# Performance work log

Measured on AMD Instinct MI355X. Metric: run time of the kernel, lower is better.

## Reference

```python
import jax, jax.numpy as jnp
import numpy as np
from jax import lax

# FPN anchor layout: 800x800 image, 3 anchors/loc, strides 4,8,16,32,64
LEVEL_ANCHORS = [120000, 30000, 7500, 1875, 507]
PRE_NMS_TOP_N = 1000   # per level (test mode)
POST_NMS_TOP_N = 1000
NMS_THRESH = 0.7
MIN_SIZE = 1e-3


def setup_inputs() -> dict:
    key = jax.random.key(0)
    k1, k2, k3, k4 = jax.random.split(key, 4)
    A = sum(LEVEL_ANCHORS)
    bs = 2
    predicts = jax.random.normal(k1, (bs, A, 4), jnp.float32) * 0.1
    objectness = jax.random.normal(k2, (bs, A, 1), jnp.float32)
    cxy = jax.random.uniform(k3, (A, 2), jnp.float32, 0.0, 800.0)
    wh = jax.random.uniform(k4, (A, 2), jnp.float32, 16.0, 128.0)
    anchors = jnp.concatenate([cxy - 0.5 * wh, cxy + 0.5 * wh], axis=-1)
    valid_size = jnp.full((bs, 2), 800.0, jnp.float32)  # (w, h) per image
    return {"predicts": predicts, "objectness": objectness,
            "anchors": anchors, "valid_size": valid_size}


def _decode(predicts, anchors):
    # BoxCoder.decoder with weights [1,1,1,1]
    awh = anchors[:, 2:] - anchors[:, :2]          # [A,2]
    axy = anchors[:, :2] + 0.5 * awh               # [A,2]
    xy = axy + predicts[..., :2] * awh             # [bs,A,2] center
    wh = jnp.exp(predicts[..., 2:]) * awh          # [bs,A,2]
    x1y1 = xy - 0.5 * wh
    return jnp.concatenate([x1y1, x1y1 + wh], axis=-1)  # [bs,A,4]


def _per_level_topk_idx(scores):
    # scores: [bs, A] -> concat of per-level top-k indices (global anchor ids)
    idx_list, offset = [], 0
    for n in LEVEL_ANCHORS:
        k = min(PRE_NMS_TOP_N, n)
        _, top = lax.top_k(scores[:, offset:offset + n], k)
        idx_list.append(top + offset)
        offset += n
    return jnp.concatenate(idx_list, axis=1)  # [bs, K]


def _nms_keep(boxes, valid, thresh):
    # boxes sorted by score desc; returns boolean keep mask (sequential NMS)
    x1, y1, x2, y2 = boxes[:, 0], boxes[:, 1], boxes[:, 2], boxes[:, 3]
    area = (x2 - x1) * (y2 - y1)
    xx1 = jnp.maximum(x1[:, None], x1[None, :])
    yy1 = jnp.maximum(y1[:, None], y1[None, :])
    xx2 = jnp.minimum(x2[:, None], x2[None, :])
    yy2 = jnp.minimum(y2[:, None], y2[None, :])
    inter = jnp.maximum(xx2 - xx1, 0.0) * jnp.maximum(yy2 - yy1, 0.0)
    iou = inter / (area[:, None] + area[None, :] - inter + 1e-9)
    sup = iou > thresh                                   # [N,N]
    N = boxes.shape[0]
    ar = jnp.arange(N)

    def body(i, keep):
        suppressed = jnp.any((ar < i) & keep & sup[i])
        return keep.at[i].set(keep[i] & ~suppressed)

    return lax.fori_loop(0, N, body, valid)


def _filter_image(boxes, scores, lvls, wh):
    # boxes [K,4], scores [K], lvls [K] int, wh [2]=(w,h)
    w, h = wh[0], wh[1]
    x1 = jnp.clip(boxes[:, 0], 0.0, w)
    y1 = jnp.clip(boxes[:, 1], 0.0, h)
    x2 = jnp.clip(boxes[:, 2], 0.0, w)
    y2 = jnp.clip(boxes[:, 3], 0.0, h)
    boxes = jnp.stack([x1, y1, x2, y2], axis=-1)
    valid = (x2 - x1 > MIN_SIZE) & (y2 - y1 > MIN_SIZE)
    s = jnp.where(valid, scores, -jnp.inf)
    order = jnp.argsort(-s)
    boxes, s, lvls, valid = boxes[order], s[order], lvls[order], valid[order]
    # batched_nms: offset each level into a disjoint coordinate range
    max_coord = lax.stop_gradient(jnp.max(boxes)) + 1.0
    off = lvls.astype(boxes.dtype) * max_coord
    keep = _nms_keep(lax.stop_gradient(boxes) + off[:, None], valid, NMS_THRESH)
    # take first POST_NMS_TOP_N kept (boxes are score-sorted)
    rank = jnp.cumsum(keep) - 1
    slot = jnp.where(keep & (rank < POST_NMS_TOP_N), rank, POST_NMS_TOP_N)
    out_b = jnp.zeros((POST_NMS_TOP_N + 1, 4), boxes.dtype).at[slot].set(boxes)[:POST_NMS_TOP_N]
    out_s = jnp.zeros((POST_NMS_TOP_N + 1,), s.dtype).at[slot].set(
        jnp.where(keep, s, 0.0))[:POST_NMS_TOP_N]
    return out_b, out_s


def reference(predicts, objectness, anchors, valid_size):
    bs = predicts.shape[0]
    proposals = _decode(predicts, anchors)            # [bs,A,4]
    scores = objectness[..., 0]                       # [bs,A]
    idx = _per_level_topk_idx(scores)                 # [bs,K]
    bidx = jnp.arange(bs)[:, None]
    boxes = proposals[bidx, idx]                      # [bs,K,4]
    sc = scores[bidx, idx]                            # [bs,K]
    levels_all = jnp.concatenate(
        [jnp.full((n,), i, jnp.int32) for i, n in enumerate(LEVEL_ANCHORS)])
    lvl = levels_all[idx]                             # [bs,K]
    final_boxes, final_scores = jax.vmap(_filter_image)(boxes, sc, lvl, valid_size)
    return final_boxes, final_scores
```

## Files before the change

### kernel.cpp

```cpp
#include <hip/hip_runtime.h>

typedef unsigned int u32;
typedef unsigned long long u64;

#define A_TOT    159882
#define BS       2
#define KTOP     1000
#define CAND_CAP 4096
#define HB       4096
#define ABLK     4096
#define NBH      40
#define EPT      16

static const size_t HIST12_OFF   = 0;
static const size_t CUT_OFF      = 131072;
static const size_t CCNT_OFF     = 131104;
static const size_t MAXC_OFF     = 131136;
static const size_t NV_OFF       = 131144;
static const size_t CHUNKANY_OFF = 131200;
static const size_t ZERO_END     = 132480;
static const size_t CAND_OFF     = 132480;
static const size_t LKEY2_OFF    = 394624;
static const size_t LBOX_OFF     = 476544;
static const size_t LSC_OFF      = 640384;
static const size_t RANK_OFF     = 681344;
static const size_t MASK_OFF     = 759168;

__device__ __forceinline__ int level_of(int a) {
  if (a < 120000) return 0;
  if (a < 150000) return 1;
  if (a < 157500) return 2;
  if (a < 159375) return 3;
  return 4;
}

__device__ __forceinline__ u32 dkey(float s) {
  u32 b = __float_as_uint(s);
  return (b & 0x80000000u) ? b : (~b & 0x7FFFFFFFu);
}

__device__ __forceinline__ void decode_clip(const float* __restrict__ pred,
                                            const float* __restrict__ anch,
                                            const float* __restrict__ vs,
                                            int b, int a,
                                            float& x1c, float& y1c, float& x2c, float& y2c,
                                            bool& valid) {
  const float* pp = pred + ((size_t)b * A_TOT + (size_t)a) * 4;
  const float* aa = anch + (size_t)a * 4;
  float ax1 = aa[0], ay1 = aa[1], ax2 = aa[2], ay2 = aa[3];
  float px = pp[0], py = pp[1], pw = pp[2], ph = pp[3];
  float aw  = __fsub_rn(ax2, ax1);
  float ah  = __fsub_rn(ay2, ay1);
  float acx = __fadd_rn(ax1, __fmul_rn(0.5f, aw));
  float acy = __fadd_rn(ay1, __fmul_rn(0.5f, ah));
  float cx  = __fadd_rn(acx, __fmul_rn(px, aw));
  float cy  = __fadd_rn(acy, __fmul_rn(py, ah));
  float w   = __fmul_rn(expf(pw), aw);
  float h   = __fmul_rn(expf(ph), ah);
  float x1  = __fsub_rn(cx, __fmul_rn(0.5f, w));
  float y1  = __fsub_rn(cy, __fmul_rn(0.5f, h));
  float x2  = __fadd_rn(x1, w);
  float y2  = __fadd_rn(y1, h);
  float Wv = vs[b * 2 + 0], Hv = vs[b * 2 + 1];
  x1c = fminf(fmaxf(x1, 0.0f), Wv);
  y1c = fminf(fmaxf(y1, 0.0f), Hv);
  x2c = fminf(fmaxf(x2, 0.0f), Wv);
  y2c = fminf(fmaxf(y2, 0.0f), Hv);
  valid = (__fsub_rn(x2c, x1c) > 0.001f) && (__fsub_rn(y2c, y1c) > 0.001f);
}

__device__ __forceinline__ void bitonic_u64(u64* arr, int N, int t, int nt) {
  for (int k = 2; k <= N; k <<= 1) {
    for (int j = k >> 1; j > 0; j >>= 1) {
      __syncthreads();
      for (int i = t; i < N; i += nt) {
        int ixj = i ^ j;
        if (ixj > i) {
          u64 x = arr[i], y = arr[ixj];
          bool up = ((i & k) == 0);
          if (up ? (x > y) : (x < y)) { arr[i] = y; arr[ixj] = x; }
        }
      }
    }
  }
  __syncthreads();
}

__device__ __forceinline__ int lbound(const u64* __restrict__ arr, int n, u64 key) {
  int lo = 0, hi = n;
  while (lo < hi) { int mid = (lo + hi) >> 1; if (arr[mid] < key) lo = mid + 1; else hi = mid; }
  return lo;
}

__global__ void k_zero(char* __restrict__ ws) {
  size_t i = (size_t)blockIdx.x * blockDim.x + threadIdx.x;
  if (i * 4 < ZERO_END) ((u32*)ws)[i] = 0u;
}

__global__ void k_hist12(const float* __restrict__ obj, char* __restrict__ ws) {
  __shared__ u32 h[2 * HB];
  int tid = threadIdx.x;
  int b = blockIdx.x / NBH, loc = blockIdx.x % NBH;
  int start = loc * ABLK;
  int l0 = level_of(start);
  if (l0 >= 4) return;
  for (int i = tid; i < 2 * HB; i += 256) h[i] = 0u;
  __syncthreads();
  for (int it = 0; it < EPT; ++it) {
    int a = start + it * 256 + tid;
    if (a < A_TOT) {
      int l = level_of(a);
      if (l < 4) {
        u32 d = dkey(obj[(size_t)b * A_TOT + a]);
        atomicAdd(&h[(u32)(l - l0) * HB + (d >> 20)], 1u);
      }
    }
  }
  __syncthreads();
  int lend = level_of(min(start + ABLK - 1, A_TOT - 1));
  int nseg = ((l0 + 1 <= lend) && (l0 + 1 < 4)) ? 2 : 1;
  for (int s = 0; s < nseg; ++s) {
    u32* gh = (u32*)(ws + HIST12_OFF) + (size_t)(b * 4 + l0 + s) * HB;
    for (int i = tid; i < HB; i += 256) {
      u32 v = h[s * HB + i];
      if (v) atomicAdd(&gh[i], v);
    }
  }
}

__global__ void k_compactsel(const float* __restrict__ obj, char* __restrict__ ws) {
  __shared__ u32 scan[256];
  __shared__ u32 cutv[2];
  __shared__ u32 lcnt[2], gbase[2];
  int tid = threadIdx.x, lane = tid & 63;
  int b = blockIdx.x / NBH, loc = blockIdx.x % NBH;
  int start = loc * ABLK;
  int l0 = level_of(start);
  if (l0 >= 4) return;
  int lend = level_of(min(start + ABLK - 1, A_TOT - 1));
  int nseg = ((l0 + 1 <= lend) && (l0 + 1 < 4)) ? 2 : 1;
  if (tid < 2) lcnt[tid] = 0;
  for (int s = 0; s < nseg; ++s) {
    int seg = b * 4 + l0 + s;
    const u32* gh = (const u32*)(ws + HIST12_OFF) + (size_t)seg * HB;
    u32 vals[16]; u32 acc = 0;
    for (int q = 0; q < 16; ++q) { vals[q] = gh[tid * 16 + q]; acc += vals[q]; }
    __syncthreads();
    scan[tid] = acc; __syncthreads();
    for (int d = 1; d < 256; d <<= 1) {
      u32 x = (tid >= d) ? scan[tid - d] : 0u; __syncthreads();
      scan[tid] += x; __syncthreads();
    }
    u32 incl = scan[tid], prev = incl - acc;
    if (prev < KTOP && incl >= KTOP) {
      u32 run = prev; int cb = HB - 1;
      for (int q = 0; q < 16; ++q) { run += vals[q]; if (run >= KTOP) { cb = tid * 16 + q; break; } }
      cutv[s] = (u32)cb;
      ((u32*)(ws + CUT_OFF))[seg] = (u32)cb;
    }
  }
  __syncthreads();
  u32 dv[EPT], slotv[EPT], passm = 0, sim = 0;
  for (int it = 0; it < EPT; ++it) {
    int a = start + it * 256 + tid;
    bool pass = false; u32 si = 0, d = 0;
    if (a < A_TOT) {
      int l = level_of(a);
      if (l < 4) {
        si = (u32)(l - l0);
        d = dkey(obj[(size_t)b * A_TOT + a]);
        pass = (d >> 20) <= cutv[si];
      }
    }
    dv[it] = d;
    u64 mp = __ballot(pass);
    u64 m1 = __ballot(pass && si == 1);
    u64 m0 = mp & ~m1;
    u32 slot = 0;
    if (m0) {
      int ld = __builtin_ctzll(m0);
      u32 wb = 0;
      if (lane == ld) wb = atomicAdd(&lcnt[0], (u32)__popcll(m0));
      wb = __shfl(wb, ld);
      if (pass && si == 0) slot = wb + (u32)__popcll(m0 & ((1ull << lane) - 1ull));
    }
    if (m1) {
      int ld = __builtin_ctzll(m1);
      u32 wb = 0;
      if (lane == ld) wb = atomicAdd(&lcnt[1], (u32)__popcll(m1));
      wb = __shfl(wb, ld);
      if (pass && si == 1) slot = wb + (u32)__popcll(m1 & ((1ull << lane) - 1ull));
    }
    slotv[it] = slot;
    if (pass) { passm |= 1u << it; if (si) sim |= 1u << it; }
  }
  __syncthreads();
  if (tid < 2)
    gbase[tid] = lcnt[tid] ? atomicAdd((u32*)(ws + CCNT_OFF) + (b * 4 + l0 + tid), lcnt[tid]) : 0u;
  __syncthreads();
  for (int it = 0; it < EPT; ++it) {
    if ((passm >> it) & 1u) {
      int a = start + it * 256 + tid;
      u32 si = (sim >> it) & 1u;
      int seg = b * 4 + l0 + (int)si;
      u32 gslot = gbase[si] + slotv[it];
      if (gslot < CAND_CAP)
        ((u64*)(ws + CAND_OFF))[(size_t)seg * CAND_CAP + gslot] =
            ((u64)dv[it] << 32) | (u32)a;
    }
  }
}

__global__ void k_sortdec(const float* __restrict__ pred, const float* __restrict__ obj,
                          const float* __restrict__ anch, const float* __restrict__ vs,
                          char* __restrict__ ws) {
  __shared__ u64 arr[CAND_CAP];
  __shared__ float4 dboxL[1024];
  __shared__ float dscL[1024];
  __shared__ u64 vmask[16];
  __shared__ u32 h8[256];
  __shared__ u32 auxv[4];
  int tid = threadIdx.x, lane = tid & 63, wv = tid >> 6;
  int P = blockIdx.x, b = P / 5, l = P % 5;
  int n;
  if (l == 4) {
    n = 507;
    for (int i = tid; i < 512; i += 256) {
      u64 v = ~0ull;
      if (i < 507) { int a = 159375 + i; v = ((u64)dkey(obj[(size_t)b * A_TOT + a]) << 32) | (u32)a; }
      arr[i] = v;
    }
    bitonic_u64(arr, 512, tid, 256);
  } else {
    n = KTOP;
    int seg = b * 4 + l;
    u32 cnt = min(((const u32*)(ws + CCNT_OFF))[seg], (u32)CAND_CAP);
    u32 cut12 = ((const u32*)(ws + CUT_OFF))[seg];
    const u64* cand = (const u64*)(ws + CAND_OFF) + (size_t)seg * CAND_CAP;
    int N;
    if (cnt <= 2048) {
      u64 ev[8];
      for (int j = 0; j < 8; ++j) { int idx = j * 256 + tid; ev[j] = (idx < (int)cnt) ? cand[idx] : ~0ull; }
      h8[tid] = 0;
      if (tid < 4) auxv[tid] = 0;
      __syncthreads();
      u32 myb = 0;
      for (int j = 0; j < 8; ++j) {
        int idx = j * 256 + tid;
        if (idx < (int)cnt) {
          u32 b12 = (u32)(ev[j] >> 52);
          if (b12 < cut12) myb++;
          else atomicAdd(&h8[(u32)(ev[j] >> 44) & 0xFFu], 1u);
        }
      }
      for (int off = 32; off; off >>= 1) myb += __shfl_xor(myb, off);
      if (lane == 0) atomicAdd(&auxv[0], myb);
      __syncthreads();
      u32 cntb = auxv[0];
      u32 hv = h8[tid];
      __syncthreads();
      for (int d = 1; d < 256; d <<= 1) {
        u32 x = (tid >= d) ? h8[tid - d] : 0u; __syncthreads();
        h8[tid] += x; __syncthreads();
      }
      u32 incl = h8[tid], excl = incl - hv;
      if (cntb + incl >= KTOP && cntb + excl < KTOP) { auxv[2] = (u32)tid; auxv[3] = cntb + incl; }
      __syncthreads();
      u32 cut20 = auxv[2]; u32 selt = auxv[3];
      for (int i = tid; i < 2048; i += 256) arr[i] = ~0ull;
      __syncthreads();
      for (int j = 0; j < 8; ++j) {
        int idx = j * 256 + tid;
        if (idx < (int)cnt) {
          u32 b12 = (u32)(ev[j] >> 52);
          bool sel = (b12 < cut12) || (((u32)(ev[j] >> 44) & 0xFFu) <= cut20);
          if (sel) { u32 p = atomicAdd(&auxv[1], 1u); arr[p] = ev[j]; }
        }
      }
      __syncthreads();
      N = 1024; while (N < (int)selt) N <<= 1;
    } else {
      for (int i = tid; i < CAND_CAP; i += 256) arr[i] = (i < (int)cnt) ? cand[i] : ~0ull;
      N = 1024; while (N < (int)cnt) N <<= 1;
    }
    bitonic_u64(arr, N, tid, 256);
  }
  float m = 0.0f;
  for (int k = 0; k < 4; ++k) {
    int j = k * 256 + tid;
    bool vb = false;
    if (j < n) {
      u64 key = arr[j];
      int a = (int)(u32)key;
      float x1, y1, x2, y2; bool valid;
      decode_clip(pred, anch, vs, b, a, x1, y1, x2, y2, valid);
      m = fmaxf(m, fmaxf(fmaxf(x1, y1), fmaxf(x2, y2)));
      dboxL[j] = make_float4(x1, y1, x2, y2);
      dscL[j] = obj[(size_t)b * A_TOT + a];
      vb = valid;
    }
    u64 bal = __ballot(vb);
    if (lane == 0) vmask[k * 4 + wv] = bal;
  }
  for (int off = 32; off; off >>= 1) m = fmaxf(m, __shfl_xor(m, off));
  if (lane == 0) atomicMax((u32*)(ws + MAXC_OFF) + b, __float_as_uint(m));
  __syncthreads();
  if (tid < 64) {
    int base = 0;
    for (int j0 = 0; j0 < n; j0 += 64) {
      int j = j0 + lane;
      bool v = (j < n) && ((vmask[j0 >> 6] >> lane) & 1ull);
      u64 mm = __ballot(v);
      int r = base + __popcll(mm & ((1ull << lane) - 1ull));
      if (v) {
        ((u64*)(ws + LKEY2_OFF))[(size_t)P * 1024 + r] = arr[j];
        ((float4*)(ws + LBOX_OFF))[(size_t)P * 1024 + r] = dboxL[j];
        ((float*)(ws + LSC_OFF))[(size_t)P * 1024 + r] = dscL[j];
      }
      base += __popcll(mm);
    }
    if (lane == 0) ((u32*)(ws + NV_OFF))[P] = (u32)base;
  }
}

__global__ void k_maskrank(char* __restrict__ ws) {
  int tid = threadIdx.x, bid = blockIdx.x;
  if (bid < 10) {
    int P = bid, b = P / 5, l = P % 5;
    int nv = (int)((const u32*)(ws + NV_OFF))[P];
    const u64* lkey = (const u64*)(ws + LKEY2_OFF);
    const u32* nvp = (const u32*)(ws + NV_OFF);
    for (int i = tid; i < nv; i += 256) {
      u64 key = lkey[(size_t)P * 1024 + i];
      int r = i;
      for (int l2 = 0; l2 < 5; ++l2) {
        if (l2 == l) continue;
        int P2 = b * 5 + l2;
        r += lbound(lkey + (size_t)P2 * 1024, (int)nvp[P2], key);
      }
      ((u32*)(ws + RANK_OFF))[(size_t)P * 1024 + i] = (u32)r;
    }
  }
  int idx = bid * 256 + tid;
  int w = idx & 15;
  int i = (idx >> 4) & 1023;
  int P = idx >> 14;
  if (P >= 10) return;
  int b = P / 5, l = P % 5;
  int n = (int)((const u32*)(ws + NV_OFF))[P];
  int W = (n + 63) >> 6;
  if (i >= n || w >= W) return;
  float M = __uint_as_float(((const u32*)(ws + MAXC_OFF))[b]);
  float maxc = __fadd_rn(M, 1.0f);
  float off = __fmul_rn((float)l, maxc);
  const float4* lbox = (const float4*)(ws + LBOX_OFF) + (size_t)P * 1024;
  float4 bi = lbox[i];
  bi.x = __fadd_rn(bi.x, off); bi.y = __fadd_rn(bi.y, off);
  bi.z = __fadd_rn(bi.z, off); bi.w = __fadd_rn(bi.w, off);
  float ai = __fmul_rn(__fsub_rn(bi.z, bi.x), __fsub_rn(bi.w, bi.y));
  u64 word = 0;
  int j0 = w << 6;
  int jn = min(64, n - j0);
  for (int jj = 0; jj < jn; ++jj) {
    float4 bj = lbox[j0 + jj];
    bj.x = __fadd_rn(bj.x, off); bj.y = __fadd_rn(bj.y, off);
    bj.z = __fadd_rn(bj.z, off); bj.w = __fadd_rn(bj.w, off);
    float xx1 = fmaxf(bi.x, bj.x);
    float yy1 = fmaxf(bi.y, bj.y);
    float xx2 = fminf(bi.z, bj.z);
    float yy2 = fminf(bi.w, bj.w);
    float iw = fmaxf(__fsub_rn(xx2, xx1), 0.0f);
    float ih = fmaxf(__fsub_rn(yy2, yy1), 0.0f);
    float inter = __fmul_rn(iw, ih);
    float aj = __fmul_rn(__fsub_rn(bj.z, bj.x), __fsub_rn(bj.w, bj.y));
    float den = __fadd_rn(__fsub_rn(__fadd_rn(ai, aj), inter), 1e-9f);
    float iou = __fdiv_rn(inter, den);
    if (iou > 0.7f) word |= (1ull << jj);
  }
  if (i >= j0 && i < j0 + 64) word &= ~(1ull << (i - j0));
  ((u64*)(ws + MASK_OFF))[(size_t)P * 16000 + (size_t)i * W + w] = word;
  if (word)
    atomicOr((u64*)(ws + CHUNKANY_OFF) + (size_t)P * 16 + (i >> 6), 1ull << (i & 63));
}

__global__ __launch_bounds__(320)
void k_scanfin(float* __restrict__ out, char* __restrict__ ws) {
  __shared__ u64 keeps[5][16];
  __shared__ u64 kb[80];
  __shared__ u32 sb[128];
  __shared__ u32 pfx[80];
  __shared__ u32 nvs[5];
  int tid = threadIdx.x, w = tid >> 6, lane = tid & 63;
  int b = blockIdx.x;
  for (int i = tid; i < 80; i += 320) kb[i] = 0ull;
  for (int i = tid; i < 4000; i += 320) out[(size_t)b * 4000 + i] = 0.0f;
  for (int i = tid; i < 1000; i += 320) out[8000 + (size_t)b * 1000 + i] = 0.0f;
  if (tid < 5) nvs[tid] = ((const u32*)(ws + NV_OFF))[b * 5 + tid];

  int P = b * 5 + w;
  int n = (int)((const u32*)(ws + NV_OFF))[P];
  int W = (n + 63) >> 6;
  const u64* maskg = (const u64*)(ws + MASK_OFF) + (size_t)P * 16000;
  u64 ca = (lane < 16) ? ((const u64*)(ws + CHUNKANY_OFF))[(size_t)P * 16 + lane] : 0ull;
  u64 dpre[16];
#pragma unroll
  for (int c = 0; c < 16; ++c) {
    int row = (c << 6) + lane;
    dpre[c] = (c < W && row < n) ? maskg[(size_t)row * W + c] : 0ull;
  }
  u64 removed = 0ull, keepw = 0ull;
#pragma unroll
  for (int c = 0; c < 16; ++c) {
    if (c >= W) break;
    int rb = c << 6;
    int rows = min(64, n - rb);
    u64 rowsmask = (rows == 64) ? ~0ull : ((1ull << rows) - 1ull);
    u64 curw = __shfl(removed, c);
    u64 cand = ~curw & rowsmask;
    u64 ca_c = __shfl(ca, c);
    u64 keptbits;
    u64 anyrows = ca_c & cand;
    if (anyrows == 0ull) {
      keptbits = cand;
    } else {
      u64 diag = dpre[c];
      u64 diagnz = __ballot(diag != 0ull) & cand;
      if (diagnz == 0ull) {
        keptbits = cand;
      } else {
        u64 remw = curw | ~rowsmask;
        u64 kept = 0ull;
        int pos = 0;
        u64 work = diagnz;
        while (work) {
          int s = __builtin_ctzll(work); work &= work - 1;
          u64 range = (1ull << s) - (1ull << pos);
          kept |= ~remw & range;
          bool k = ((remw >> s) & 1ull) == 0ull;
          u64 dr = __shfl(diag, s);
          if (k) { kept |= 1ull << s; remw |= dr; }
          pos = s + 1;
        }
        u64 tail = (pos >= 64) ? 0ull : (~0ull << pos);
        kept |= ~remw & tail & rowsmask;
        keptbits = kept;
      }
      u64 todo = keptbits & ca_c;
      while (todo) {
        int r0 = __builtin_ctzll(todo); todo &= todo - 1;
        int r1 = -1, r2 = -1, r3 = -1;
        if (todo) { r1 = __builtin_ctzll(todo); todo &= todo - 1; }
        if (todo) { r2 = __builtin_ctzll(todo); todo &= todo - 1; }
        if (todo) { r3 = __builtin_ctzll(todo); todo &= todo - 1; }
        u64 v0 = 0, v1 = 0, v2 = 0, v3 = 0;
        if (lane < W) {
          v0 = maskg[(size_t)(rb + r0) * W + lane];
          if (r1 >= 0) v1 = maskg[(size_t)(rb + r1) * W + lane];
          if (r2 >= 0) v2 = maskg[(size_t)(rb + r2) * W + lane];
          if (r3 >= 0) v3 = maskg[(size_t)(rb + r3) * W + lane];
        }
        removed |= v0 | v1 | v2 | v3;
      }
    }
    if (lane == c) keepw |= keptbits;
  }
  if (lane < 16) keeps[w][lane] = keepw;
  __syncthreads();

  const u32* rank = (const u32*)(ws + RANK_OFF);
  for (int idx = tid; idx < 5120; idx += 320) {
    int p = idx >> 10, i = idx & 1023;
    if (i < (int)nvs[p] && ((keeps[p][i >> 6] >> (i & 63)) & 1ull)) {
      u32 r = rank[(size_t)(b * 5 + p) * 1024 + i];
      atomicOr(&kb[r >> 6], 1ull << (r & 63));
    }
  }
  __syncthreads();
  if (tid < 128) sb[tid] = (tid < 80) ? (u32)__popcll(kb[tid]) : 0u;
  __syncthreads();
  for (int d = 1; d < 128; d <<= 1) {
    u32 x = (tid < 128 && tid >= d) ? sb[tid - d] : 0u;
    __syncthreads();
    if (tid < 128) sb[tid] += x;
    __syncthreads();
  }
  if (tid < 80) pfx[tid] = sb[tid] - (u32)__popcll(kb[tid]);
  __syncthreads();
  for (int idx = tid; idx < 5120; idx += 320) {
    int p = idx >> 10, i = idx & 1023;
    if (i < (int)nvs[p] && ((keeps[p][i >> 6] >> (i & 63)) & 1ull)) {
      int Pp = b * 5 + p;
      u32 r = rank[(size_t)Pp * 1024 + i];
      u64 word = kb[r >> 6];
      int slot = (int)pfx[r >> 6] + __popcll(word & ((1ull << (r & 63)) - 1ull));
      if (slot < KTOP) {
        float4 bx = ((const float4*)(ws + LBOX_OFF))[(size_t)Pp * 1024 + i];
        float s = ((const float*)(ws + LSC_OFF))[(size_t)Pp * 1024 + i];
        float* ob = out + ((size_t)b * KTOP + slot) * 4;
        ob[0] = bx.x; ob[1] = bx.y; ob[2] = bx.z; ob[3] = bx.w;
        out[8000 + (size_t)b * KTOP + slot] = s;
      }
    }
  }
}

extern "C" void kernel_launch(void* const* d_in, const int* in_sizes, int n_in,
                              void* d_out, int out_size, void* d_ws, size_t ws_size,
                              hipStream_t stream) {
  const float* pred = (const float*)d_in[0];
  const float* obj  = (const float*)d_in[1];
  const float* anch = (const float*)d_in[2];
  const float* vs   = (const float*)d_in[3];
  float* out = (float*)d_out;
  char* ws = (char*)d_ws;
  (void)in_sizes; (void)n_in; (void)out_size; (void)ws_size;

  int gZ = (int)((ZERO_END / 4 + 255) / 256);
  k_zero      <<<gZ,        256, 0, stream>>>(ws);
  k_hist12    <<<BS * NBH,  256, 0, stream>>>(obj, ws);
  k_compactsel<<<BS * NBH,  256, 0, stream>>>(obj, ws);
  k_sortdec   <<<10,        256, 0, stream>>>(pred, obj, anch, vs, ws);
  k_maskrank  <<<640,       256, 0, stream>>>(ws);
  k_scanfin   <<<2,         320, 0, stream>>>(out, ws);
}
```

Measured before the change: 194.6 us.

## Replace shared-memory bitonic with register/shuffle bitonic sort of 2048 keys

The per-level candidate sort in k_sortdec now keeps 8 keys per thread in registers. It uses in-register compare-swaps for small strides, wavefront shuffles for mid strides and shared memory only for strides of 512 and above. This replaces the histogram-based prefilter and the shared-memory bitonic sort, cutting barriers and LDS traffic. The trade-off is that every segment with at most 2048 candidates now always sorts a full 2048 elements, and the last level pads 507 keys to 2048, which adds compare work.

Measured after the change: 193.8 us. No clear change (-0.4%).

```diff
diff --git a/kernel.cpp b/kernel.cpp
--- a/kernel.cpp
+++ b/kernel.cpp
@@ -86,10 +86,58 @@
   __syncthreads();
 }
 
-__device__ __forceinline__ int lbound(const u64* __restrict__ arr, int n, u64 key) {
-  int lo = 0, hi = n;
-  while (lo < hi) { int mid = (lo + hi) >> 1; if (arr[mid] < key) lo = mid + 1; else hi = mid; }
-  return lo;
+__device__ __forceinline__ u64 shfl_xor_u64(u64 x, int lanemask) {
+  u32 lo = (u32)x, hi = (u32)(x >> 32);
+  lo = (u32)__shfl_xor((int)lo, lanemask);
+  hi = (u32)__shfl_xor((int)hi, lanemask);
+  return ((u64)hi << 32) | (u64)lo;
+}
+
+__device__ __forceinline__ void regsort2048(u64 v[8], int tid, u64* arr) {
+  for (int k = 2; k <= 2048; k <<= 1) {
+    for (int j = k >> 1; j > 0; j >>= 1) {
+      if (j >= 512) {
+        __syncthreads();
+#pragma unroll
+        for (int e = 0; e < 8; ++e) arr[tid * 8 + e] = v[e];
+        __syncthreads();
+#pragma unroll
+        for (int e = 0; e < 8; ++e) {
+          int i = tid * 8 + e, p = i ^ j;
+          u64 o = arr[p];
+          bool up = ((i & k) == 0);
+          bool keepmin = ((i < p) == up);
+          v[e] = keepmin ? (v[e] < o ? v[e] : o) : (v[e] > o ? v[e] : o);
+        }
+      } else if (j >= 8) {
+        int dl = j >> 3;
+#pragma unroll
+        for (int e = 0; e < 8; ++e) {
+          int i = tid * 8 + e;
+          u64 o = shfl_xor_u64(v[e], dl);
+          bool up = ((i & k) == 0);
+          bool keepmin = (((tid & dl) == 0) == up);
+          v[e] = keepmin ? (v[e] < o ? v[e] : o) : (v[e] > o ? v[e] : o);
+        }
+      } else {
+#pragma unroll
+        for (int e = 0; e < 8; ++e) {
+          int pe = e ^ j;
+          if (pe > e) {
+            int i = tid * 8 + e;
+            bool up = ((i & k) == 0);
+            u64 a = v[e], b2 = v[pe];
+            bool sw = up ? (a > b2) : (a < b2);
+            if (sw) { v[e] = b2; v[pe] = a; }
+          }
+        }
+      }
+    }
+  }
+  __syncthreads();
+#pragma unroll
+  for (int e = 0; e < 8; ++e) arr[tid * 8 + e] = v[e];
+  __syncthreads();
 }
 
 __global__ void k_zero(char* __restrict__ ws) {
@@ -218,72 +266,39 @@
   __shared__ float4 dboxL[1024];
   __shared__ float dscL[1024];
   __shared__ u64 vmask[16];
-  __shared__ u32 h8[256];
-  __shared__ u32 auxv[4];
   int tid = threadIdx.x, lane = tid & 63, wv = tid >> 6;
   int P = blockIdx.x, b = P / 5, l = P % 5;
   int n;
   if (l == 4) {
     n = 507;
-    for (int i = tid; i < 512; i += 256) {
-      u64 v = ~0ull;
-      if (i < 507) { int a = 159375 + i; v = ((u64)dkey(obj[(size_t)b * A_TOT + a]) << 32) | (u32)a; }
-      arr[i] = v;
-    }
-    bitonic_u64(arr, 512, tid, 256);
+    u64 v[8];
+#pragma unroll
+    for (int e = 0; e < 8; ++e) {
+      int idx = tid * 8 + e;
+      if (idx < 507) {
+        int a = 159375 + idx;
+        v[e] = ((u64)dkey(obj[(size_t)b * A_TOT + a]) << 32) | (u32)a;
+      } else v[e] = ~0ull;
+    }
+    regsort2048(v, tid, arr);
   } else {
     n = KTOP;
     int seg = b * 4 + l;
     u32 cnt = min(((const u32*)(ws + CCNT_OFF))[seg], (u32)CAND_CAP);
-    u32 cut12 = ((const u32*)(ws + CUT_OFF))[seg];
     const u64* cand = (const u64*)(ws + CAND_OFF) + (size_t)seg * CAND_CAP;
-    int N;
     if (cnt <= 2048) {
-      u64 ev[8];
-      for (int j = 0; j < 8; ++j) { int idx = j * 256 + tid; ev[j] = (idx < (int)cnt) ? cand[idx] : ~0ull; }
-      h8[tid] = 0;
-      if (tid < 4) auxv[tid] = 0;
-      __syncthreads();
-      u32 myb = 0;
-      for (int j = 0; j < 8; ++j) {
-        int idx = j * 256 + tid;
-        if (idx < (int)cnt) {
-          u32 b12 = (u32)(ev[j] >> 52);
-          if (b12 < cut12) myb++;
-          else atomicAdd(&h8[(u32)(ev[j] >> 44) & 0xFFu], 1u);
-        }
-      }
-      for (int off = 32; off; off >>= 1) myb += __shfl_xor(myb, off);
-      if (lane == 0) atomicAdd(&auxv[0], myb);
-      __syncthreads();
-      u32 cntb = auxv[0];
-      u32 hv = h8[tid];
-      __syncthreads();
-      for (int d = 1; d < 256; d <<= 1) {
-        u32 x = (tid >= d) ? h8[tid - d] : 0u; __syncthreads();
-        h8[tid] += x; __syncthreads();
-      }
-      u32 incl = h8[tid], excl = incl - hv;
-      if (cntb + incl >= KTOP && cntb + excl < KTOP) { auxv[2] = (u32)tid; auxv[3] = cntb + incl; }
-      __syncthreads();
-      u32 cut20 = auxv[2]; u32 selt = auxv[3];
-      for (int i = tid; i < 2048; i += 256) arr[i] = ~0ull;
-      __syncthreads();
-      for (int j = 0; j < 8; ++j) {
-        int idx = j * 256 + tid;
-        if (idx < (int)cnt) {
-          u32 b12 = (u32)(ev[j] >> 52);
-          bool sel = (b12 < cut12) || (((u32)(ev[j] >> 44) & 0xFFu) <= cut20);
-          if (sel) { u32 p = atomicAdd(&auxv[1], 1u); arr[p] = ev[j]; }
-        }
-      }
-      __syncthreads();
-      N = 1024; while (N < (int)selt) N <<= 1;
+      u64 v[8];
+#pragma unroll
+      for (int e = 0; e < 8; ++e) {
+        int idx = tid * 8 + e;
+        v[e] = (idx < (int)cnt) ? cand[idx] : ~0ull;
+      }
+      regsort2048(v, tid, arr);
     } else {
       for (int i = tid; i < CAND_CAP; i += 256) arr[i] = (i < (int)cnt) ? cand[i] : ~0ull;
-      N = 1024; while (N < (int)cnt) N <<= 1;
-    }
-    bitonic_u64(arr, N, tid, 256);
+      int N = 2048; while (N < (int)cnt) N <<= 1;
+      bitonic_u64(arr, N, tid, 256);
+    }
   }
   float m = 0.0f;
   for (int k = 0; k < 4; ++k) {
@@ -321,6 +336,12 @@
     }
     if (lane == 0) ((u32*)(ws + NV_OFF))[P] = (u32)base;
   }
+}
+
+__device__ __forceinline__ int lbound(const u64* __restrict__ arr, int n, u64 key) {
+  int lo = 0, hi = n;
+  while (lo < hi) { int mid = (lo + hi) >> 1; if (arr[mid] < key) lo = mid + 1; else hi = mid; }
+  return lo;
 }
 
 __global__ void k_maskrank(char* __restrict__ ws) {
```
